# Performance work log

Hardware: AMD Instinct MI355X
Metric: run time of the kernel (lower is better)

## Reference

```python
import jax, jax.numpy as jnp
import numpy as np

N_NODES = 100000
N_EDGES = 500000
D_IN = 128
D_HID = 256
D_OUT = 1


def mish(x):
    # x * tanh(softplus(x))
    return x * jnp.tanh(jax.nn.softplus(x))


def setup_inputs() -> dict:
    key = jax.random.key(0)
    k1, k2, k3, k4, k5, k6 = jax.random.split(key, 6)
    z = jax.random.normal(k1, (N_NODES, D_IN), dtype=jnp.float32)
    edge = jax.random.randint(k2, (2, N_EDGES), 0, N_NODES, dtype=jnp.int64)
    # PyTorch Linear default init: U(-1/sqrt(fan_in), 1/sqrt(fan_in))
    s1 = 1.0 / np.sqrt(D_IN)
    s2 = 1.0 / np.sqrt(D_HID)
    W1 = jax.random.uniform(k3, (D_HID, D_IN), minval=-s1, maxval=s1, dtype=jnp.float32)
    b1 = jax.random.uniform(k4, (D_HID,), minval=-s1, maxval=s1, dtype=jnp.float32)
    W2 = jax.random.uniform(k5, (D_OUT, D_HID), minval=-s2, maxval=s2, dtype=jnp.float32)
    b2 = jax.random.uniform(k6, (D_OUT,), minval=-s2, maxval=s2, dtype=jnp.float32)
    return {"z": z, "edge": edge, "W1": W1, "b1": b1, "W2": W2, "b2": b2}


def reference(z, edge, W1, b1, W2, b2):
    # gather node pairs and elementwise product: [E, D_IN]
    x = z[edge[0]] * z[edge[1]]
    # fc1 + mish (dropout is identity in eval mode)
    h = mish(jnp.einsum('ed,hd->eh', x, W1) + b1)
    # fc2 + sigmoid -> [E, 1]
    logits = jnp.einsum('eh,oh->eo', h, W2) + b2
    return jax.nn.sigmoid(logits)
```

## Files before the change

kernel.cpp:

```cpp
#include <hip/hip_runtime.h>
#include <hip/hip_bf16.h>


#define N_EDGES 500000
#define D_IN    128
#define D_HID   256
#define M_TILE  32
#define NTILES  (N_EDGES / M_TILE)
#define LDS_STRIDE 136
#define GRID    512

typedef __bf16 bf16x8 __attribute__((ext_vector_type(8)));
typedef float  f32x4  __attribute__((ext_vector_type(4)));
typedef float  f32x2  __attribute__((ext_vector_type(2)));

union F4H { float4 v; f32x2 h[2]; };

__device__ __forceinline__ unsigned int pkbf(f32x2 q) {
    union { __hip_bfloat162 b; unsigned int u; } c;
    c.b = __float22bfloat162_rn(make_float2(q.x, q.y));
    return c.u;
}

__device__ __forceinline__ f32x2 mish2(f32x2 x) {
    f32x2 xc = {fminf(x.x, 20.0f), fminf(x.y, 20.0f)};
    f32x2 E  = {__expf(xc.x), __expf(xc.y)};
    f32x2 num = E * (E + 2.0f);
    f32x2 den = num + 2.0f;
    f32x2 r  = {__builtin_amdgcn_rcpf(den.x), __builtin_amdgcn_rcpf(den.y)};
    return x * num * r;
}

__global__ __launch_bounds__(512, 4)
void edge_decoder_kernel(const float* __restrict__ z,
                         const int*   __restrict__ edge,
                         const float* __restrict__ W1,
                         const float* __restrict__ b1,
                         const float* __restrict__ W2,
                         const float* __restrict__ b2,
                         float*       __restrict__ out) {
    __shared__ ushort xbuf[2][M_TILE * LDS_STRIDE];
    __shared__ float  lpart[2][8][M_TILE];

    const int t    = threadIdx.x;
    const int wave = t >> 6;
    const int lane = t & 63;
    const int quad = lane >> 4;
    const int nlo  = lane & 15;

    bf16x8 bfrag[4][2];
    float  b1f[2], w2f[2];
    #pragma unroll
    for (int nt = 0; nt < 2; ++nt) {
        const int n = wave * 32 + nt * 16 + nlo;
        const float* wrow = W1 + n * D_IN;
        #pragma unroll
        for (int ks = 0; ks < 4; ++ks) {
            F4H w0, w1;
            w0.v = *reinterpret_cast<const float4*>(wrow + ks * 32 + quad * 8);
            w1.v = *reinterpret_cast<const float4*>(wrow + ks * 32 + quad * 8 + 4);
            union { unsigned int u[4]; bf16x8 v; } o;
            o.u[0] = pkbf(w0.h[0]); o.u[1] = pkbf(w0.h[1]);
            o.u[2] = pkbf(w1.h[0]); o.u[3] = pkbf(w1.h[1]);
            bfrag[ks][nt] = o.v;
        }
        b1f[nt] = b1[n];
        w2f[nt] = W2[n];
    }
    const float b2f = b2[0];

    const int s_slot = t >> 4;
    const int cch    = t & 15;

    int tile = blockIdx.x;
    float4 a0, a1, c0, c1;
    {
        const int e = tile * M_TILE + s_slot;
        const int u = edge[e], v = edge[N_EDGES + e];
        const float* zu = z + (size_t)u * D_IN + cch * 8;
        const float* zv = z + (size_t)v * D_IN + cch * 8;
        a0 = *reinterpret_cast<const float4*>(zu);
        a1 = *reinterpret_cast<const float4*>(zu + 4);
        c0 = *reinterpret_cast<const float4*>(zv);
        c1 = *reinterpret_cast<const float4*>(zv + 4);
    }
    int u_n, v_n;
    {
        const int t1 = min(tile + GRID, NTILES - 1);
        const int e1 = t1 * M_TILE + s_slot;
        u_n = edge[e1]; v_n = edge[N_EDGES + e1];
    }

    int  p = 0;
    bool have_prev = false;
    int  prev_base = 0;

    for (; tile < NTILES; tile += GRID) {
        {
            F4H A0{a0}, A1{a1}, C0{c0}, C1{c1};
            unsigned int r0 = pkbf(A0.h[0] * C0.h[0]);
            unsigned int r1 = pkbf(A0.h[1] * C0.h[1]);
            unsigned int r2 = pkbf(A1.h[0] * C1.h[0]);
            unsigned int r3 = pkbf(A1.h[1] * C1.h[1]);
            *reinterpret_cast<uint4*>(&xbuf[p][s_slot * LDS_STRIDE + cch * 8]) =
                make_uint4(r0, r1, r2, r3);
        }
        __syncthreads();

        {
            const float* zu = z + (size_t)u_n * D_IN + cch * 8;
            const float* zv = z + (size_t)v_n * D_IN + cch * 8;
            a0 = *reinterpret_cast<const float4*>(zu);
            a1 = *reinterpret_cast<const float4*>(zu + 4);
            c0 = *reinterpret_cast<const float4*>(zv);
            c1 = *reinterpret_cast<const float4*>(zv + 4);
        }
        {
            const int t2 = min(tile + 2 * GRID, NTILES - 1);
            const int e2 = t2 * M_TILE + s_slot;
            u_n = edge[e2]; v_n = edge[N_EDGES + e2];
        }

        if (have_prev) {
            if (t < M_TILE) {
                const int pp = p ^ 1;
                float logit = b2f;
                #pragma unroll
                for (int w = 0; w < 8; ++w) logit += lpart[pp][w][t];
                out[prev_base + t] = __builtin_amdgcn_rcpf(1.0f + __expf(-logit));
            }
        }

        f32x4 acc[2][2];
        #pragma unroll
        for (int mt = 0; mt < 2; ++mt)
            #pragma unroll
            for (int nt = 0; nt < 2; ++nt)
                acc[mt][nt] = (f32x4){0.f, 0.f, 0.f, 0.f};

        #pragma unroll
        for (int ks = 0; ks < 4; ++ks) {
            bf16x8 af[2];
            #pragma unroll
            for (int mt = 0; mt < 2; ++mt)
                af[mt] = *reinterpret_cast<const bf16x8*>(
                    &xbuf[p][(mt * 16 + nlo) * LDS_STRIDE + ks * 32 + quad * 8]);
            #pragma unroll
            for (int mt = 0; mt < 2; ++mt)
                #pragma unroll
                for (int nt = 0; nt < 2; ++nt)
                    acc[mt][nt] = __builtin_amdgcn_mfma_f32_16x16x32_bf16(
                        af[mt], bfrag[ks][nt], acc[mt][nt], 0, 0, 0);
        }

        #pragma unroll
        for (int mt = 0; mt < 2; ++mt) {
            #pragma unroll
            for (int pr = 0; pr < 2; ++pr) {
                f32x2 s2 = {0.f, 0.f};
                #pragma unroll
                for (int nt = 0; nt < 2; ++nt) {
                    f32x2 h = {acc[mt][nt][2 * pr]     + b1f[nt],
                               acc[mt][nt][2 * pr + 1] + b1f[nt]};
                    f32x2 m = mish2(h);
                    s2.x += m.x * w2f[nt];
                    s2.y += m.y * w2f[nt];
                }
                float sx = s2.x, sy = s2.y;
                sx += __shfl_xor(sx, 1); sy += __shfl_xor(sy, 1);
                sx += __shfl_xor(sx, 2); sy += __shfl_xor(sy, 2);
                sx += __shfl_xor(sx, 4); sy += __shfl_xor(sy, 4);
                sx += __shfl_xor(sx, 8); sy += __shfl_xor(sy, 8);
                if (nlo == 0) {
                    const int row = mt * 16 + quad * 4 + pr * 2;
                    lpart[p][wave][row]     = sx;
                    lpart[p][wave][row + 1] = sy;
                }
            }
        }

        have_prev = true;
        prev_base = tile * M_TILE;
        p ^= 1;
    }

    __syncthreads();
    if (have_prev && t < M_TILE) {
        const int pp = p ^ 1;
        float logit = b2f;
        #pragma unroll
        for (int w = 0; w < 8; ++w) logit += lpart[pp][w][t];
        out[prev_base + t] = __builtin_amdgcn_rcpf(1.0f + __expf(-logit));
    }
}

extern "C" void kernel_launch(void* const* d_in, const int* in_sizes, int n_in,
                              void* d_out, int out_size, void* d_ws, size_t ws_size,
                              hipStream_t stream) {
    const float* z    = (const float*)d_in[0];
    const int*   edge = (const int*)d_in[1];
    const float* W1   = (const float*)d_in[2];
    const float* b1   = (const float*)d_in[3];
    const float* W2   = (const float*)d_in[4];
    const float* b2   = (const float*)d_in[5];
    float* out = (float*)d_out;

    edge_decoder_kernel<<<dim3(GRID), dim3(512), 0, stream>>>(z, edge, W1, b1, W2, b2, out);
}
```

Measured before the change: 176.2 us.

## Pre-convert node features to fp16 and gather half-precision rows into f16 MFMA

Adds a pre-pass kernel that converts z to fp16 in the workspace, so the edge kernel gathers half-size rows and multiplies them directly in fp16 before f16 MFMAs. This targets the random-gather bandwidth that dominates the edge decoder. It also doubles the grid and raises the occupancy hint in launch bounds. The cost is an extra full pass over z (read fp32, write fp16) each call, and fp16 products in place of bf16 may lose range.

Result: slower. 325.8 us (+84.9%).

```diff
diff --git a/kernel.cpp b/kernel.cpp
--- a/kernel.cpp
+++ b/kernel.cpp
@@ -1,18 +1,22 @@
 #include <hip/hip_runtime.h>
 #include <hip/hip_bf16.h>
-
-
+#include <hip/hip_fp16.h>
+#include <type_traits>
+
+
+#define N_NODES 100000
 #define N_EDGES 500000
 #define D_IN    128
 #define D_HID   256
 #define M_TILE  32
 #define NTILES  (N_EDGES / M_TILE)
 #define LDS_STRIDE 136
-#define GRID    512
-
-typedef __bf16 bf16x8 __attribute__((ext_vector_type(8)));
-typedef float  f32x4  __attribute__((ext_vector_type(4)));
-typedef float  f32x2  __attribute__((ext_vector_type(2)));
+#define GRID    1024
+
+typedef _Float16 half8  __attribute__((ext_vector_type(8)));
+typedef __bf16   bf16x8 __attribute__((ext_vector_type(8)));
+typedef float    f32x4  __attribute__((ext_vector_type(4)));
+typedef float    f32x2  __attribute__((ext_vector_type(2)));
 
 union F4H { float4 v; f32x2 h[2]; };
 
@@ -31,14 +35,31 @@
     return x * num * r;
 }
 
-__global__ __launch_bounds__(512, 4)
-void edge_decoder_kernel(const float* __restrict__ z,
-                         const int*   __restrict__ edge,
-                         const float* __restrict__ W1,
-                         const float* __restrict__ b1,
-                         const float* __restrict__ W2,
-                         const float* __restrict__ b2,
-                         float*       __restrict__ out) {
+__global__ __launch_bounds__(256)
+void zcvt_kernel(const float* __restrict__ z, _Float16* __restrict__ zh) {
+    const size_t i = (size_t)blockIdx.x * 256 + threadIdx.x;
+    const float4 f0 = *reinterpret_cast<const float4*>(z + i * 8);
+    const float4 f1 = *reinterpret_cast<const float4*>(z + i * 8 + 4);
+    union { half8 h; uint4 u; } o;
+    o.h[0] = (_Float16)f0.x; o.h[1] = (_Float16)f0.y;
+    o.h[2] = (_Float16)f0.z; o.h[3] = (_Float16)f0.w;
+    o.h[4] = (_Float16)f1.x; o.h[5] = (_Float16)f1.y;
+    o.h[6] = (_Float16)f1.z; o.h[7] = (_Float16)f1.w;
+    *reinterpret_cast<uint4*>(zh + i * 8) = o.u;
+}
+
+template <bool USE_H>
+__global__ __launch_bounds__(512, 8)
+void edge_decoder_kernel(const float*    __restrict__ z,
+                         const _Float16* __restrict__ zh,
+                         const int*      __restrict__ edge,
+                         const float*    __restrict__ W1,
+                         const float*    __restrict__ b1,
+                         const float*    __restrict__ W2,
+                         const float*    __restrict__ b2,
+                         float*          __restrict__ out) {
+    using frag_t = std::conditional_t<USE_H, half8, bf16x8>;
+
     __shared__ ushort xbuf[2][M_TILE * LDS_STRIDE];
     __shared__ float  lpart[2][8][M_TILE];
 
@@ -48,7 +69,7 @@
     const int quad = lane >> 4;
     const int nlo  = lane & 15;
 
-    bf16x8 bfrag[4][2];
+    frag_t bfrag[4][2];
     float  b1f[2], w2f[2];
     #pragma unroll
     for (int nt = 0; nt < 2; ++nt) {
@@ -56,13 +77,20 @@
         const float* wrow = W1 + n * D_IN;
         #pragma unroll
         for (int ks = 0; ks < 4; ++ks) {
-            F4H w0, w1;
-            w0.v = *reinterpret_cast<const float4*>(wrow + ks * 32 + quad * 8);
-            w1.v = *reinterpret_cast<const float4*>(wrow + ks * 32 + quad * 8 + 4);
-            union { unsigned int u[4]; bf16x8 v; } o;
-            o.u[0] = pkbf(w0.h[0]); o.u[1] = pkbf(w0.h[1]);
-            o.u[2] = pkbf(w1.h[0]); o.u[3] = pkbf(w1.h[1]);
-            bfrag[ks][nt] = o.v;
+            float4 w0 = *reinterpret_cast<const float4*>(wrow + ks * 32 + quad * 8);
+            float4 w1 = *reinterpret_cast<const float4*>(wrow + ks * 32 + quad * 8 + 4);
+            float wa[8] = {w0.x, w0.y, w0.z, w0.w, w1.x, w1.y, w1.z, w1.w};
+            if constexpr (USE_H) {
+                half8 hv;
+                #pragma unroll
+                for (int j = 0; j < 8; ++j) hv[j] = (_Float16)wa[j];
+                bfrag[ks][nt] = hv;
+            } else {
+                bf16x8 bv;
+                #pragma unroll
+                for (int j = 0; j < 8; ++j) bv[j] = (__bf16)wa[j];
+                bfrag[ks][nt] = bv;
+            }
         }
         b1f[nt] = b1[n];
         w2f[nt] = W2[n];
@@ -74,15 +102,21 @@
 
     int tile = blockIdx.x;
     float4 a0, a1, c0, c1;
+    half8  ha, hc;
     {
         const int e = tile * M_TILE + s_slot;
         const int u = edge[e], v = edge[N_EDGES + e];
-        const float* zu = z + (size_t)u * D_IN + cch * 8;
-        const float* zv = z + (size_t)v * D_IN + cch * 8;
-        a0 = *reinterpret_cast<const float4*>(zu);
-        a1 = *reinterpret_cast<const float4*>(zu + 4);
-        c0 = *reinterpret_cast<const float4*>(zv);
-        c1 = *reinterpret_cast<const float4*>(zv + 4);
+        if constexpr (USE_H) {
+            ha = *reinterpret_cast<const half8*>(zh + (size_t)u * D_IN + cch * 8);
+            hc = *reinterpret_cast<const half8*>(zh + (size_t)v * D_IN + cch * 8);
+        } else {
+            const float* zu = z + (size_t)u * D_IN + cch * 8;
+            const float* zv = z + (size_t)v * D_IN + cch * 8;
+            a0 = *reinterpret_cast<const float4*>(zu);
+            a1 = *reinterpret_cast<const float4*>(zu + 4);
+            c0 = *reinterpret_cast<const float4*>(zv);
+            c1 = *reinterpret_cast<const float4*>(zv + 4);
+        }
     }
     int u_n, v_n;
     {
@@ -96,7 +130,11 @@
     int  prev_base = 0;
 
     for (; tile < NTILES; tile += GRID) {
-        {
+        if constexpr (USE_H) {
+            union { half8 h; uint4 u; } pr;
+            pr.h = ha * hc;
+            *reinterpret_cast<uint4*>(&xbuf[p][s_slot * LDS_STRIDE + cch * 8]) = pr.u;
+        } else {
             F4H A0{a0}, A1{a1}, C0{c0}, C1{c1};
             unsigned int r0 = pkbf(A0.h[0] * C0.h[0]);
             unsigned int r1 = pkbf(A0.h[1] * C0.h[1]);
@@ -107,7 +145,10 @@
         }
         __syncthreads();
 
-        {
+        if constexpr (USE_H) {
+            ha = *reinterpret_cast<const half8*>(zh + (size_t)u_n * D_IN + cch * 8);
+            hc = *reinterpret_cast<const half8*>(zh + (size_t)v_n * D_IN + cch * 8);
+        } else {
             const float* zu = z + (size_t)u_n * D_IN + cch * 8;
             const float* zv = z + (size_t)v_n * D_IN + cch * 8;
             a0 = *reinterpret_cast<const float4*>(zu);
@@ -140,17 +181,22 @@
 
         #pragma unroll
         for (int ks = 0; ks < 4; ++ks) {
-            bf16x8 af[2];
+            frag_t af[2];
             #pragma unroll
             for (int mt = 0; mt < 2; ++mt)
-                af[mt] = *reinterpret_cast<const bf16x8*>(
+                af[mt] = *reinterpret_cast<const frag_t*>(
                     &xbuf[p][(mt * 16 + nlo) * LDS_STRIDE + ks * 32 + quad * 8]);
             #pragma unroll
             for (int mt = 0; mt < 2; ++mt)
                 #pragma unroll
-                for (int nt = 0; nt < 2; ++nt)
-                    acc[mt][nt] = __builtin_amdgcn_mfma_f32_16x16x32_bf16(
-                        af[mt], bfrag[ks][nt], acc[mt][nt], 0, 0, 0);
+                for (int nt = 0; nt < 2; ++nt) {
+                    if constexpr (USE_H)
+                        acc[mt][nt] = __builtin_amdgcn_mfma_f32_16x16x32_f16(
+                            af[mt], bfrag[ks][nt], acc[mt][nt], 0, 0, 0);
+                    else
+                        acc[mt][nt] = __builtin_amdgcn_mfma_f32_16x16x32_bf16(
+                            af[mt], bfrag[ks][nt], acc[mt][nt], 0, 0, 0);
+                }
         }
 
         #pragma unroll
@@ -205,5 +251,14 @@
     const float* b2   = (const float*)d_in[5];
     float* out = (float*)d_out;
 
-    edge_decoder_kernel<<<dim3(GRID), dim3(512), 0, stream>>>(z, edge, W1, b1, W2, b2, out);
-}
+    const size_t zh_bytes = (size_t)N_NODES * D_IN * sizeof(_Float16);
+    if (d_ws != nullptr && ws_size >= zh_bytes) {
+        _Float16* zh = (_Float16*)d_ws;
+        zcvt_kernel<<<dim3(N_NODES * D_IN / 8 / 256), dim3(256), 0, stream>>>(z, zh);
+        edge_decoder_kernel<true><<<dim3(GRID), dim3(512), 0, stream>>>(
+            z, zh, edge, W1, b1, W2, b2, out);
+    } else {
+        edge_decoder_kernel<false><<<dim3(GRID), dim3(512), 0, stream>>>(
+            z, nullptr, edge, W1, b1, W2, b2, out);
+    }
+}
```
